# Optimization experiments

Measured on AMD Instinct MI355X. Metric: run time of the kernel, lower is better.

The kernel has to match this reference:

```python
import jax, jax.numpy as jnp
import numpy as np

N = 8192
E = 524288
IN_DIM = 128
HID = 256
OUT_DIM = 128
N_LAYERS = 3
N_HEADS = 4
HEAD_DIM = HID // N_HEADS


def setup_inputs() -> dict:
    key = jax.random.key(0)
    ks = jax.random.split(key, 12)
    s = 0.05
    return {
        "x": jax.random.normal(ks[0], (N, IN_DIM), dtype=jnp.float32),
        "edge_index": jax.random.randint(ks[1], (2, E), 0, N, dtype=jnp.int64),
        "W_in": jax.random.normal(ks[2], (HID, IN_DIM), dtype=jnp.float32) * s,
        "b_in": jnp.zeros((HID,), dtype=jnp.float32),
        "plasticity": jnp.ones((N_LAYERS,), dtype=jnp.float32),
        "synaptic": jnp.ones((N_LAYERS,), dtype=jnp.float32),
        "in_proj_w": jax.random.normal(ks[3], (3 * HID, HID), dtype=jnp.float32) * s,
        "in_proj_b": jnp.zeros((3 * HID,), dtype=jnp.float32),
        "out_proj_w": jax.random.normal(ks[4], (HID, HID), dtype=jnp.float32) * s,
        "out_proj_b": jnp.zeros((HID,), dtype=jnp.float32),
        "W_out": jax.random.normal(ks[5], (OUT_DIM, HID), dtype=jnp.float32) * s,
        "b_out": jnp.zeros((OUT_DIM,), dtype=jnp.float32),
    }


def _forward(x, edge_index, W_in, b_in, plasticity, synaptic,
             in_proj_w, in_proj_b, out_proj_w, out_proj_b, W_out, b_out):
    src, dst = edge_index[0], edge_index[1]  # x_j = x[src], aggregate at dst (source_to_target)
    x = x @ W_in.T + b_in  # [N, HID]
    for i in range(N_LAYERS):
        x = x * jax.nn.sigmoid(plasticity[i])
        # message: x_j * sigmoid(synaptic) (scalar edge weight); aggr='add'
        agg = jax.ops.segment_sum(x[src], dst, num_segments=N)  # gather-scatter-add
        x = jax.nn.leaky_relu(agg * jax.nn.sigmoid(synaptic[i]), negative_slope=0.01)
    # MultiheadAttention over all N nodes (seq_len=N, batch=1)
    qkv = x @ in_proj_w.T + in_proj_b  # [N, 3*HID]
    q, k, v = jnp.split(qkv, 3, axis=-1)
    q = q.reshape(N, N_HEADS, HEAD_DIM).transpose(1, 0, 2)  # [h, n, d]
    k = k.reshape(N, N_HEADS, HEAD_DIM).transpose(1, 0, 2)
    v = v.reshape(N, N_HEADS, HEAD_DIM).transpose(1, 0, 2)
    scores = jnp.einsum("hnd,hmd->hnm", q, k) / np.sqrt(HEAD_DIM).astype(np.float32)
    attn = jax.nn.softmax(scores, axis=-1)
    o = jnp.einsum("hnm,hmd->hnd", attn, v)  # [h, n, d]
    o = o.transpose(1, 0, 2).reshape(N, HID)
    x = o @ out_proj_w.T + out_proj_b
    return x @ W_out.T + b_out  # [N, OUT_DIM]


def reference(x, edge_index, W_in, b_in, plasticity, synaptic,
              in_proj_w, in_proj_b, out_proj_w, out_proj_b, W_out, b_out):
    return _forward(x, edge_index, W_in, b_in, plasticity, synaptic,
                    in_proj_w, in_proj_b, out_proj_w, out_proj_b, W_out, b_out)
```

## Files before the change

### kernel.cpp

```cpp
#include <hip/hip_runtime.h>
#include <hip/hip_bf16.h>
#include <float.h>

#define N_NODES 8192
#define NEDGE   524288
#define IND     128
#define HID     256
#define OUTD    128
#define NHEAD   4
#define HD      64

typedef short short8 __attribute__((ext_vector_type(8)));
typedef short short4v __attribute__((ext_vector_type(4)));
typedef float f32x4  __attribute__((ext_vector_type(4)));
typedef float f32x16 __attribute__((ext_vector_type(16)));
typedef unsigned int u32x4 __attribute__((ext_vector_type(4)));

__device__ __forceinline__ float sigmoidf_(float x) { return 1.0f / (1.0f + expf(-x)); }

__device__ __forceinline__ unsigned short f2bf(float f) {
    __hip_bfloat16 b = __float2bfloat16(f);
    return __builtin_bit_cast(unsigned short, b);
}
__device__ __forceinline__ float bf2f(unsigned short u) {
    __hip_bfloat16 b = __builtin_bit_cast(__hip_bfloat16, u);
    return __bfloat162float(b);
}
__device__ __forceinline__ void split3(float x, unsigned short& a, unsigned short& b, unsigned short& c) {
    a = f2bf(x); float r = x - bf2f(a);
    b = f2bf(r); r = r - bf2f(b);
    c = f2bf(r);
}
__device__ __forceinline__ void split2(float x, unsigned short& a, unsigned short& b) {
    a = f2bf(x); float r = x - bf2f(a);
    b = f2bf(r);
}
__device__ __forceinline__ unsigned int cvtpk(float lo, float hi) {
    unsigned int r;
    asm("v_cvt_pk_bf16_f32 %0, %1, %2" : "=v"(r) : "v"(lo), "v"(hi));
    return r;
}
__device__ __forceinline__ void plswap(unsigned int& a, unsigned int& b) {
    asm volatile("v_permlane32_swap_b32 %0, %1" : "+v"(a), "+v"(b));
}
__device__ __forceinline__ void gll16(const void* g, void* l) {
    __builtin_amdgcn_global_load_lds(
        (const __attribute__((address_space(1))) void*)g,
        (__attribute__((address_space(3))) void*)l, 16, 0, 0);
}
__device__ __forceinline__ f32x16 mfma32(short8 a, short8 b, f32x16 c) {
    return __builtin_amdgcn_mfma_f32_32x32x16_bf16(a, b, c, 0, 0, 0);
}

__global__ void hist_kernel(const int* __restrict__ ei, int* __restrict__ deg)
{
    int e = blockIdx.x * blockDim.x + threadIdx.x;
    if (e < NEDGE) atomicAdd(&deg[ei[NEDGE + e]], 1);
}

__global__ __launch_bounds__(1024) void scan_kernel(
    const int* __restrict__ deg, int* __restrict__ row_ptr, int* __restrict__ cursor)
{
    __shared__ int sh[1024];
    const int t = threadIdx.x;
    int v[8]; int s = 0;
    #pragma unroll
    for (int i = 0; i < 8; ++i) { v[i] = deg[t * 8 + i]; s += v[i]; }
    sh[t] = s; __syncthreads();
    for (int off = 1; off < 1024; off <<= 1) {
        int add = (t >= off) ? sh[t - off] : 0;
        __syncthreads();
        sh[t] += add;
        __syncthreads();
    }
    int base = sh[t] - s;
    #pragma unroll
    for (int i = 0; i < 8; ++i) {
        row_ptr[t * 8 + i] = base;
        cursor[t * 8 + i]  = base;
        base += v[i];
    }
    if (t == 1023) row_ptr[N_NODES] = base;
}

__global__ void scatter_kernel(const int* __restrict__ ei, int* __restrict__ cursor,
                               int* __restrict__ esrc)
{
    int e = blockIdx.x * blockDim.x + threadIdx.x;
    if (e < NEDGE) {
        int d = ei[NEDGE + e];
        int p = atomicAdd(&cursor[d], 1);
        esrc[p] = ei[e];
    }
}

__global__ __launch_bounds__(256) void split_x_kernel(
    const float* __restrict__ x,
    unsigned short* __restrict__ X0, unsigned short* __restrict__ X1,
    unsigned short* __restrict__ X2)
{
    const int i = (blockIdx.x * 256 + threadIdx.x) * 8;
    float4 a = *(const float4*)(x + i);
    float4 b = *(const float4*)(x + i + 4);
    float v[8] = {a.x, a.y, a.z, a.w, b.x, b.y, b.z, b.w};
    short8 c0, c1, c2;
    #pragma unroll
    for (int j = 0; j < 8; ++j) {
        unsigned short p, q, r;
        split3(v[j], p, q, r);
        c0[j] = (short)p; c1[j] = (short)q; c2[j] = (short)r;
    }
    *(short8*)(X0 + i) = c0;
    *(short8*)(X1 + i) = c1;
    *(short8*)(X2 + i) = c2;
}

__global__ __launch_bounds__(256) void aggregate_kernel(
    const float* __restrict__ hin, float* __restrict__ hout,
    const int* __restrict__ row_ptr, const int* __restrict__ esrc,
    const float* __restrict__ plas, const float* __restrict__ syn, int layer)
{
    const int b = blockIdx.x;
    const int c = threadIdx.x;
    const int st = row_ptr[b], en = row_ptr[b + 1];
    float a0 = 0.f, a1 = 0.f, a2 = 0.f, a3 = 0.f;
    int e = st;
    for (; e + 4 <= en; e += 4) {
        int s0 = esrc[e], s1 = esrc[e + 1], s2 = esrc[e + 2], s3 = esrc[e + 3];
        a0 += hin[(size_t)s0 * HID + c];
        a1 += hin[(size_t)s1 * HID + c];
        a2 += hin[(size_t)s2 * HID + c];
        a3 += hin[(size_t)s3 * HID + c];
    }
    float acc = (a0 + a1) + (a2 + a3);
    for (; e < en; ++e) acc += hin[(size_t)esrc[e] * HID + c];
    const float scale = sigmoidf_(plas[layer]) * sigmoidf_(syn[layer]);
    float x = acc * scale;
    hout[(size_t)b * HID + c] = (x > 0.f) ? x : 0.01f * x;
}

__global__ __launch_bounds__(256) void aggregate_split_kernel(
    const float* __restrict__ hin,
    unsigned short* __restrict__ H0, unsigned short* __restrict__ H1,
    unsigned short* __restrict__ H2,
    const int* __restrict__ row_ptr, const int* __restrict__ esrc,
    const float* __restrict__ plas, const float* __restrict__ syn, int layer)
{
    const int b = blockIdx.x;
    const int c = threadIdx.x;
    const int st = row_ptr[b], en = row_ptr[b + 1];
    float a0 = 0.f, a1 = 0.f, a2 = 0.f, a3 = 0.f;
    int e = st;
    for (; e + 4 <= en; e += 4) {
        int s0 = esrc[e], s1 = esrc[e + 1], s2 = esrc[e + 2], s3 = esrc[e + 3];
        a0 += hin[(size_t)s0 * HID + c];
        a1 += hin[(size_t)s1 * HID + c];
        a2 += hin[(size_t)s2 * HID + c];
        a3 += hin[(size_t)s3 * HID + c];
    }
    float acc = (a0 + a1) + (a2 + a3);
    for (; e < en; ++e) acc += hin[(size_t)esrc[e] * HID + c];
    const float scale = sigmoidf_(plas[layer]) * sigmoidf_(syn[layer]);
    float x = acc * scale;
    x = (x > 0.f) ? x : 0.01f * x;
    unsigned short p, q, r;
    split3(x, p, q, r);
    H0[(size_t)b * HID + c] = p;
    H1[(size_t)b * HID + c] = q;
    H2[(size_t)b * HID + c] = r;
}

template<int NT, int NA, bool SOUT>
__global__ __launch_bounds__(256) void mfma_gemm_kernel(
    const unsigned short* __restrict__ A0, const unsigned short* __restrict__ A1,
    const unsigned short* __restrict__ A2,
    const float* __restrict__ W, const float* __restrict__ bias,
    float* __restrict__ Cf, unsigned short* __restrict__ C0, unsigned short* __restrict__ C1,
    int M, int Nn, int K)
{
    const int t = threadIdx.x;
    const int wv = t >> 6, lane = t & 63;
    const int l31 = lane & 31, l5 = lane >> 5;
    const int wm = wv & 1, wn = wv >> 1;
    const int m0 = blockIdx.x * 64 + wm * 32;
    const int n0 = blockIdx.y * 64 + wn * 32;
    const int mrow = m0 + l31;
    const int nrow = n0 + l31;

    f32x16 o;
    #pragma unroll
    for (int r = 0; r < 16; ++r) o[r] = 0.f;

    for (int k = 0; k < K; k += 16) {
        const int kk = k + l5 * 8;
        short8 af[NA];
        af[0] = *(const short8*)(A0 + (size_t)mrow * K + kk);
        af[1] = *(const short8*)(A1 + (size_t)mrow * K + kk);
        if (NA > 2) af[2] = *(const short8*)(A2 + (size_t)mrow * K + kk);
        const float* wp = W + (size_t)nrow * K + kk;
        float4 w4a = *(const float4*)wp, w4b = *(const float4*)(wp + 4);
        float wvle[8] = {w4a.x, w4a.y, w4a.z, w4a.w, w4b.x, w4b.y, w4b.z, w4b.w};
        short8 wf[3];
        #pragma unroll
        for (int j = 0; j < 8; ++j) {
            if (NT == 6) {
                unsigned short a, b, c;
                split3(wvle[j], a, b, c);
                wf[0][j] = (short)a; wf[1][j] = (short)b; wf[2][j] = (short)c;
            } else {
                unsigned short a, b;
                split2(wvle[j], a, b);
                wf[0][j] = (short)a; wf[1][j] = (short)b;
            }
        }
        if (NT == 6) {
            o = mfma32(wf[0], af[2], o);
            o = mfma32(wf[1], af[1], o);
            o = mfma32(wf[2], af[0], o);
            o = mfma32(wf[0], af[1], o);
            o = mfma32(wf[1], af[0], o);
            o = mfma32(wf[0], af[0], o);
        } else {
            o = mfma32(wf[0], af[1], o);
            o = mfma32(wf[1], af[0], o);
            o = mfma32(wf[0], af[0], o);
        }
    }

    #pragma unroll
    for (int g = 0; g < 4; ++g) {
        const int nb = n0 + g * 8 + l5 * 4;
        const float4 b4 = *(const float4*)(bias + nb);
        float v0 = o[4 * g + 0] + b4.x;
        float v1 = o[4 * g + 1] + b4.y;
        float v2 = o[4 * g + 2] + b4.z;
        float v3 = o[4 * g + 3] + b4.w;
        if (!SOUT) {
            float4 st = {v0, v1, v2, v3};
            *(float4*)(Cf + (size_t)mrow * Nn + nb) = st;
        } else {
            unsigned short h0, h1, p0, p1, q0, q1, r0, r1;
            split2(v0, h0, h1); split2(v1, p0, p1);
            split2(v2, q0, q1); split2(v3, r0, r1);
            short4v s0 = {(short)h0, (short)p0, (short)q0, (short)r0};
            short4v s1 = {(short)h1, (short)p1, (short)q1, (short)r1};
            *(short4v*)(C0 + (size_t)mrow * Nn + nb) = s0;
            *(short4v*)(C1 + (size_t)mrow * Nn + nb) = s1;
        }
    }
}

__global__ __launch_bounds__(256) void split_kernel(
    const float* __restrict__ qkv,
    unsigned short* __restrict__ Kc0, unsigned short* __restrict__ Kc1,
    unsigned short* __restrict__ Kc2, unsigned short* __restrict__ Vt0)
{
    __shared__ unsigned short vts[64 * 80];
    const int h  = blockIdx.y;
    const int n0 = blockIdx.x * 64;
    const int t  = threadIdx.x;
    const int r  = t >> 2;
    const int n  = n0 + r;
    const int dc = (t & 3) * 16;

    {
        const float* kp = qkv + (size_t)n * 768 + 256 + h * 64 + dc;
        float kv[16];
        #pragma unroll
        for (int i = 0; i < 16; i += 4) {
            float4 f = *(const float4*)(kp + i);
            kv[i] = f.x; kv[i+1] = f.y; kv[i+2] = f.z; kv[i+3] = f.w;
        }
        #pragma unroll
        for (int half = 0; half < 2; ++half) {
            short8 c0, c1, c2;
            #pragma unroll
            for (int j = 0; j < 8; ++j) {
                unsigned short a, b, c;
                split3(kv[half * 8 + j], a, b, c);
                c0[j] = (short)a; c1[j] = (short)b; c2[j] = (short)c;
            }
            const int pos = ((dc >> 3) + half) ^ (n & 7);
            const size_t base = ((size_t)(h * 8192 + n)) * 64 + pos * 8;
            *(short8*)(Kc0 + base) = c0;
            *(short8*)(Kc1 + base) = c1;
            *(short8*)(Kc2 + base) = c2;
        }
    }
    {
        const float* vp = qkv + (size_t)n * 768 + 512 + h * 64 + dc;
        #pragma unroll
        for (int i = 0; i < 16; i += 4) {
            float4 f = *(const float4*)(vp + i);
            float vv[4] = {f.x, f.y, f.z, f.w};
            #pragma unroll
            for (int k2 = 0; k2 < 4; ++k2)
                vts[(dc + i + k2) * 80 + r] = f2bf(vv[k2]);
        }
    }
    __syncthreads();
    #pragma unroll
    for (int i = 0; i < 2; ++i) {
        const int q = t * 2 + i;
        const int d = q >> 3, nc = q & 7;
        const int g = nc >> 2, c = nc & 3;
        short8 vv = *(const short8*)(&vts[d * 80 + nc * 8]);
        const size_t dst = ((size_t)(h * 64 + d)) * 8192 + n0 + g * 32 + ((c ^ (d & 3)) * 8);
        *(short8*)(Vt0 + dst) = vv;
    }
}

__global__ __launch_bounds__(256, 3) void attn_mfma_kernel(
    const float* __restrict__ qkv,
    const unsigned short* __restrict__ Kc0, const unsigned short* __restrict__ Kc1,
    const unsigned short* __restrict__ Kc2, const unsigned short* __restrict__ Vt0,
    unsigned short* __restrict__ Op16, float* __restrict__ Ml)
{
    __shared__ __align__(16) char smem[32768];
    const int h    = blockIdx.y;
    const int quar = blockIdx.z;
    const int n0   = blockIdx.x * 128;
    const int t    = threadIdx.x;
    const int wv   = t >> 6;
    const int lane = t & 63;
    const int l31  = lane & 31, l5 = lane >> 5;
    const int qbase = n0 + wv * 32;

    const float QSC = 0.125f * 1.4426950408889634f;
    short8 qf[3][4];
    #pragma unroll
    for (int ks = 0; ks < 4; ++ks) {
        const float* qp = qkv + (size_t)(qbase + l31) * 768 + h * 64 + ks * 16 + l5 * 8;
        float4 qa = *(const float4*)qp, qb4 = *(const float4*)(qp + 4);
        float qv[8] = {qa.x, qa.y, qa.z, qa.w, qb4.x, qb4.y, qb4.z, qb4.w};
        #pragma unroll
        for (int j = 0; j < 8; ++j) {
            unsigned short a, b, c;
            split3(qv[j] * QSC, a, b, c);
            qf[0][ks][j] = (short)a;
            qf[1][ks][j] = (short)b;
            qf[2][ks][j] = (short)c;
        }
    }

    const char* sgb[4];
    int ldso[4];
    #pragma unroll
    for (int i = 0; i < 4; ++i) {
        const int s = wv * 4 + i;
        if (s < 12) {
            const int c = s >> 2, rb = s & 3;
            const unsigned short* base = (c == 0) ? Kc0 : (c == 1) ? Kc1 : Kc2;
            const int row = rb * 8 + (lane >> 3);
            sgb[i] = (const char*)(base + ((size_t)(h * 8192 + quar * 2048 + row)) * 64 + (lane & 7) * 8);
            ldso[i] = c * 4096 + rb * 1024;
        } else {
            const int v = s - 12;
            const int d = v * 16 + (lane >> 2);
            sgb[i] = (const char*)(Vt0 + ((size_t)(h * 64 + d)) * 8192 + quar * 2048 + (lane & 3) * 8);
            ldso[i] = 12288 + v * 1024;
        }
    }
    const size_t ktstride = (wv < 3) ? 4096 : 64;

    auto STAGE = [&](int kt, int bb) {
        #pragma unroll
        for (int i = 0; i < 4; ++i)
            gll16(sgb[i] + (size_t)kt * ktstride, &smem[bb * 16384 + ldso[i]]);
    };

    f32x16 o[2];
    #pragma unroll
    for (int db = 0; db < 2; ++db)
        #pragma unroll
        for (int r = 0; r < 16; ++r) o[db][r] = 0.f;
    float mr = -FLT_MAX, ls = 0.f;

    STAGE(0, 0);
    __syncthreads();

    for (int kt = 0; kt < 64; ++kt) {
        const int bb = kt & 1;
        if (kt < 63) STAGE(kt + 1, bb ^ 1);
        const char* buf = &smem[bb * 16384];

        f32x16 s;
        #pragma unroll
        for (int r = 0; r < 16; ++r) s[r] = 0.f;

        __builtin_amdgcn_s_setprio(1);
        #pragma unroll
        for (int ks = 0; ks < 4; ++ks) {
            const int off = l31 * 128 + (((ks * 2 + l5) ^ (l31 & 7)) * 16);
            short8 k0 = *(const short8*)(buf + off);
            short8 k1 = *(const short8*)(buf + 4096 + off);
            short8 k2 = *(const short8*)(buf + 8192 + off);
            s = mfma32(k0, qf[2][ks], s);
            s = mfma32(k1, qf[1][ks], s);
            s = mfma32(k2, qf[0][ks], s);
            s = mfma32(k0, qf[1][ks], s);
            s = mfma32(k1, qf[0][ks], s);
            s = mfma32(k0, qf[0][ks], s);
        }
        __builtin_amdgcn_s_setprio(0);

        float mx = s[0];
        #pragma unroll
        for (int r = 1; r < 16; ++r) mx = fmaxf(mx, s[r]);
        mx = fmaxf(mx, __shfl_xor(mx, 32));
        if (__any(mx > mr + 12.0f)) {
            const float mn = fmaxf(mr, mx);
            const float alpha = exp2f(mr - mn);
            mr = mn;
            ls *= alpha;
            o[0] *= alpha;
            o[1] *= alpha;
        }
        float ps = 0.f;
        #pragma unroll
        for (int r = 0; r < 16; ++r) {
            float p = exp2f(s[r] - mr);
            s[r] = p;
            ps += p;
        }
        ps += __shfl_xor(ps, 32);
        ls += ps;

        short8 pb[2];
        #pragma unroll
        for (int ks = 0; ks < 2; ++ks) {
            const int rb = ks * 8;
            unsigned int A0 = cvtpk(s[rb + 0], s[rb + 1]);
            unsigned int A1 = cvtpk(s[rb + 2], s[rb + 3]);
            unsigned int B0 = cvtpk(s[rb + 4], s[rb + 5]);
            unsigned int B1 = cvtpk(s[rb + 6], s[rb + 7]);
            plswap(A0, B0);
            plswap(A1, B1);
            u32x4 pw; pw[0] = A0; pw[1] = A1; pw[2] = B0; pw[3] = B1;
            pb[ks] = __builtin_bit_cast(short8, pw);
        }

        __builtin_amdgcn_s_setprio(1);
        #pragma unroll
        for (int ks = 0; ks < 2; ++ks) {
            #pragma unroll
            for (int db = 0; db < 2; ++db) {
                const int d = db * 32 + l31;
                const int off = 12288 + d * 64 + (((ks * 2 + l5) ^ (d & 3)) * 16);
                short8 v = *(const short8*)(buf + off);
                o[db] = mfma32(v, pb[ks], o[db]);
            }
        }
        __builtin_amdgcn_s_setprio(0);

        __syncthreads();
    }

    {
        const int q = qbase + l31;
        unsigned short* opq = Op16 + ((size_t)((quar * 4 + h) * 8192 + q)) * 64;
        #pragma unroll
        for (int db = 0; db < 2; ++db) {
            #pragma unroll
            for (int tq = 0; tq < 4; ++tq) {
                const int d0 = db * 32 + tq * 8 + l5 * 4;
                unsigned int w0 = cvtpk(o[db][4 * tq + 0], o[db][4 * tq + 1]);
                unsigned int w1 = cvtpk(o[db][4 * tq + 2], o[db][4 * tq + 3]);
                uint2 st = {w0, w1};
                *(uint2*)(opq + d0) = st;
            }
        }
        if (l5 == 0) {
            Ml[((size_t)(quar * 4 + h) * 2 + 0) * 8192 + q] = mr;
            Ml[((size_t)(quar * 4 + h) * 2 + 1) * 8192 + q] = ls;
        }
    }
}

__global__ __launch_bounds__(256) void combine_kernel(
    const unsigned short* __restrict__ Op16, const float* __restrict__ Ml,
    unsigned short* __restrict__ aO0, unsigned short* __restrict__ aO1)
{
    const int idx = blockIdx.x * 256 + threadIdx.x;
    const int c = idx & 3;
    const int q = (idx >> 2) & 8191;
    const int h = idx >> 15;
    float m[4], l[4];
    float mg = -FLT_MAX;
    #pragma unroll
    for (int s = 0; s < 4; ++s) {
        m[s] = Ml[((size_t)(s * 4 + h) * 2 + 0) * 8192 + q];
        l[s] = Ml[((size_t)(s * 4 + h) * 2 + 1) * 8192 + q];
        mg = fmaxf(mg, m[s]);
    }
    float w[4], denom = 0.f;
    #pragma unroll
    for (int s = 0; s < 4; ++s) {
        w[s] = exp2f(m[s] - mg);
        denom += l[s] * w[s];
    }
    const float inv = 1.f / denom;
    float acc[16] = {};
    #pragma unroll
    for (int s = 0; s < 4; ++s) {
        const unsigned short* p = Op16 + ((size_t)(s * 4 + h) * 8192 + q) * 64 + c * 16;
        short8 v0 = *(const short8*)(p);
        short8 v1 = *(const short8*)(p + 8);
        #pragma unroll
        for (int i = 0; i < 8; ++i) {
            acc[i]     += w[s] * bf2f((unsigned short)v0[i]);
            acc[i + 8] += w[s] * bf2f((unsigned short)v1[i]);
        }
    }
    unsigned short* d0 = aO0 + (size_t)q * 256 + h * 64 + c * 16;
    unsigned short* d1 = aO1 + (size_t)q * 256 + h * 64 + c * 16;
    short8 o0, o1;
    #pragma unroll
    for (int i = 0; i < 8; ++i) {
        unsigned short a, b;
        split2(acc[i] * inv, a, b);
        o0[i] = (short)a; o1[i] = (short)b;
    }
    *(short8*)(d0) = o0;
    *(short8*)(d1) = o1;
    #pragma unroll
    for (int i = 0; i < 8; ++i) {
        unsigned short a, b;
        split2(acc[i + 8] * inv, a, b);
        o0[i] = (short)a; o1[i] = (short)b;
    }
    *(short8*)(d0 + 8) = o0;
    *(short8*)(d1 + 8) = o1;
}

extern "C" void kernel_launch(void* const* d_in, const int* in_sizes, int n_in,
                              void* d_out, int out_size, void* d_ws, size_t ws_size,
                              hipStream_t stream)
{
    const float* x     = (const float*)d_in[0];
    const int*   ei    = (const int*)  d_in[1];
    const float* W_in  = (const float*)d_in[2];
    const float* b_in  = (const float*)d_in[3];
    const float* plas  = (const float*)d_in[4];
    const float* syn   = (const float*)d_in[5];
    const float* inpw  = (const float*)d_in[6];
    const float* inpb  = (const float*)d_in[7];
    const float* outpw = (const float*)d_in[8];
    const float* outpb = (const float*)d_in[9];
    const float* Wout  = (const float*)d_in[10];
    const float* bout  = (const float*)d_in[11];
    float* out = (float*)d_out;

    char* ws = (char*)d_ws;
    float* h    = (float*)(ws + 0);
    float* h2   = (float*)(ws + (8u  << 20));
    float* qkv  = (float*)(ws + (16u << 20));
    unsigned short* xc0  = (unsigned short*)(ws + (16u << 20));
    unsigned short* xc1  = (unsigned short*)(ws + (18u << 20));
    unsigned short* xc2  = (unsigned short*)(ws + (20u << 20));
    unsigned short* h2c0 = (unsigned short*)(ws + (8u  << 20));
    unsigned short* h2c1 = (unsigned short*)(ws + (12u << 20));
    unsigned short* h2c2 = (unsigned short*)(ws + (40u << 20));
    unsigned short* Kc0  = (unsigned short*)(ws + 0);
    unsigned short* Kc1  = (unsigned short*)(ws + (4u  << 20));
    unsigned short* Kc2  = (unsigned short*)(ws + (8u  << 20));
    unsigned short* Vt0  = (unsigned short*)(ws + (12u << 20));
    unsigned short* Op16 = (unsigned short*)(ws + (40u << 20));
    unsigned short* aOc0 = (unsigned short*)(ws + 0);
    unsigned short* aOc1 = (unsigned short*)(ws + (4u  << 20));
    unsigned short* tmpc0 = (unsigned short*)(ws + (8u  << 20));
    unsigned short* tmpc1 = (unsigned short*)(ws + (12u << 20));
    int*   rowp = (int*)(ws + (56u << 20));
    int*   curs = (int*)(ws + (56u << 20) + 40960);
    int*   esrc = (int*)(ws + (56u << 20) + 81920);
    float* Ml   = (float*)(ws + (56u << 20) + 81920);

    hipMemsetAsync(curs, 0, N_NODES * sizeof(int), stream);
    hist_kernel<<<NEDGE / 256, 256, 0, stream>>>(ei, curs);
    scan_kernel<<<1, 1024, 0, stream>>>(curs, rowp, curs);
    scatter_kernel<<<NEDGE / 256, 256, 0, stream>>>(ei, curs, esrc);

    split_x_kernel<<<(N_NODES * IND) / (256 * 8), 256, 0, stream>>>(x, xc0, xc1, xc2);
    mfma_gemm_kernel<6, 3, false><<<dim3(N_NODES / 64, HID / 64), 256, 0, stream>>>(
        xc0, xc1, xc2, W_in, b_in, h, nullptr, nullptr, N_NODES, HID, IND);

    aggregate_kernel<<<N_NODES, 256, 0, stream>>>(h,  h2, rowp, esrc, plas, syn, 0);
    aggregate_kernel<<<N_NODES, 256, 0, stream>>>(h2, h,  rowp, esrc, plas, syn, 1);
    aggregate_split_kernel<<<N_NODES, 256, 0, stream>>>(h, h2c0, h2c1, h2c2,
                                                        rowp, esrc, plas, syn, 2);

    mfma_gemm_kernel<6, 3, false><<<dim3(N_NODES / 64, 768 / 64), 256, 0, stream>>>(
        h2c0, h2c1, h2c2, inpw, inpb, qkv, nullptr, nullptr, N_NODES, 768, HID);

    split_kernel<<<dim3(N_NODES / 64, NHEAD), 256, 0, stream>>>(
        qkv, Kc0, Kc1, Kc2, Vt0);

    attn_mfma_kernel<<<dim3(N_NODES / 128, NHEAD, 4), 256, 0, stream>>>(
        qkv, Kc0, Kc1, Kc2, Vt0, Op16, Ml);

    combine_kernel<<<512, 256, 0, stream>>>(Op16, Ml, aOc0, aOc1);

    mfma_gemm_kernel<3, 2, true><<<dim3(N_NODES / 64, HID / 64), 256, 0, stream>>>(
        aOc0, aOc1, nullptr, outpw, outpb, nullptr, tmpc0, tmpc1, N_NODES, HID, HID);
    mfma_gemm_kernel<3, 2, false><<<dim3(N_NODES / 64, OUTD / 64), 256, 0, stream>>>(
        tmpc0, tmpc1, nullptr, Wout, bout, out, nullptr, nullptr, N_NODES, OUTD, HID);
}
```

Before: 602.7 us.

## Pre-split weights into bf16 parts, slice aggregation by column, hoist attention offsets

Weights are now split once into bf16 hi/mid/lo planes by a dedicated kernel before each GEMM, so GEMM blocks stop re-splitting fp32 weights inside the K loop. The aggregation kernels remap blocks so each block handles 4 destination nodes over a 64-column slice, with blocks interleaved across halves of the node range, aiming for better cache locality on gathers. The attention kernel precomputes swizzled LDS offsets outside its loop and raises the launch-bounds occupancy hint from 3 to 4, which may increase register pressure. Extra small split launches are added and the split planes use extra workspace regions.

```diff
diff --git a/kernel.cpp b/kernel.cpp
--- a/kernel.cpp
+++ b/kernel.cpp
@@ -94,14 +94,13 @@
     }
 }
 
-__global__ __launch_bounds__(256) void split_x_kernel(
-    const float* __restrict__ x,
-    unsigned short* __restrict__ X0, unsigned short* __restrict__ X1,
-    unsigned short* __restrict__ X2)
+__global__ __launch_bounds__(256) void split_w_kernel(
+    const float* __restrict__ w, unsigned short* __restrict__ Wc, int elems)
 {
     const int i = (blockIdx.x * 256 + threadIdx.x) * 8;
-    float4 a = *(const float4*)(x + i);
-    float4 b = *(const float4*)(x + i + 4);
+    if (i >= elems) return;
+    float4 a = *(const float4*)(w + i);
+    float4 b = *(const float4*)(w + i + 4);
     float v[8] = {a.x, a.y, a.z, a.w, b.x, b.y, b.z, b.w};
     short8 c0, c1, c2;
     #pragma unroll
@@ -110,36 +109,40 @@
         split3(v[j], p, q, r);
         c0[j] = (short)p; c1[j] = (short)q; c2[j] = (short)r;
     }
-    *(short8*)(X0 + i) = c0;
-    *(short8*)(X1 + i) = c1;
-    *(short8*)(X2 + i) = c2;
-}
-
-__global__ __launch_bounds__(256) void aggregate_kernel(
+    *(short8*)(Wc + i) = c0;
+    *(short8*)(Wc + elems + i) = c1;
+    *(short8*)(Wc + 2 * elems + i) = c2;
+}
+
+__global__ __launch_bounds__(256) void aggregate_sliced_kernel(
     const float* __restrict__ hin, float* __restrict__ hout,
     const int* __restrict__ row_ptr, const int* __restrict__ esrc,
     const float* __restrict__ plas, const float* __restrict__ syn, int layer)
 {
     const int b = blockIdx.x;
-    const int c = threadIdx.x;
-    const int st = row_ptr[b], en = row_ptr[b + 1];
+    const int xs = b & 7, g = b >> 3;
+    const int slice = xs & 3, halfn = xs >> 2;
+    const int t = threadIdx.x;
+    const int dst = halfn * 4096 + g * 4 + (t >> 6);
+    const int col = slice * 64 + (t & 63);
+    const int st = row_ptr[dst], en = row_ptr[dst + 1];
     float a0 = 0.f, a1 = 0.f, a2 = 0.f, a3 = 0.f;
     int e = st;
     for (; e + 4 <= en; e += 4) {
         int s0 = esrc[e], s1 = esrc[e + 1], s2 = esrc[e + 2], s3 = esrc[e + 3];
-        a0 += hin[(size_t)s0 * HID + c];
-        a1 += hin[(size_t)s1 * HID + c];
-        a2 += hin[(size_t)s2 * HID + c];
-        a3 += hin[(size_t)s3 * HID + c];
+        a0 += hin[(size_t)s0 * HID + col];
+        a1 += hin[(size_t)s1 * HID + col];
+        a2 += hin[(size_t)s2 * HID + col];
+        a3 += hin[(size_t)s3 * HID + col];
     }
     float acc = (a0 + a1) + (a2 + a3);
-    for (; e < en; ++e) acc += hin[(size_t)esrc[e] * HID + c];
+    for (; e < en; ++e) acc += hin[(size_t)esrc[e] * HID + col];
     const float scale = sigmoidf_(plas[layer]) * sigmoidf_(syn[layer]);
     float x = acc * scale;
-    hout[(size_t)b * HID + c] = (x > 0.f) ? x : 0.01f * x;
-}
-
-__global__ __launch_bounds__(256) void aggregate_split_kernel(
+    hout[(size_t)dst * HID + col] = (x > 0.f) ? x : 0.01f * x;
+}
+
+__global__ __launch_bounds__(256) void aggregate_sliced_split_kernel(
     const float* __restrict__ hin,
     unsigned short* __restrict__ H0, unsigned short* __restrict__ H1,
     unsigned short* __restrict__ H2,
@@ -147,34 +150,38 @@
     const float* __restrict__ plas, const float* __restrict__ syn, int layer)
 {
     const int b = blockIdx.x;
-    const int c = threadIdx.x;
-    const int st = row_ptr[b], en = row_ptr[b + 1];
+    const int xs = b & 7, g = b >> 3;
+    const int slice = xs & 3, halfn = xs >> 2;
+    const int t = threadIdx.x;
+    const int dst = halfn * 4096 + g * 4 + (t >> 6);
+    const int col = slice * 64 + (t & 63);
+    const int st = row_ptr[dst], en = row_ptr[dst + 1];
     float a0 = 0.f, a1 = 0.f, a2 = 0.f, a3 = 0.f;
     int e = st;
     for (; e + 4 <= en; e += 4) {
         int s0 = esrc[e], s1 = esrc[e + 1], s2 = esrc[e + 2], s3 = esrc[e + 3];
-        a0 += hin[(size_t)s0 * HID + c];
-        a1 += hin[(size_t)s1 * HID + c];
-        a2 += hin[(size_t)s2 * HID + c];
-        a3 += hin[(size_t)s3 * HID + c];
+        a0 += hin[(size_t)s0 * HID + col];
+        a1 += hin[(size_t)s1 * HID + col];
+        a2 += hin[(size_t)s2 * HID + col];
+        a3 += hin[(size_t)s3 * HID + col];
     }
     float acc = (a0 + a1) + (a2 + a3);
-    for (; e < en; ++e) acc += hin[(size_t)esrc[e] * HID + c];
+    for (; e < en; ++e) acc += hin[(size_t)esrc[e] * HID + col];
     const float scale = sigmoidf_(plas[layer]) * sigmoidf_(syn[layer]);
     float x = acc * scale;
     x = (x > 0.f) ? x : 0.01f * x;
     unsigned short p, q, r;
     split3(x, p, q, r);
-    H0[(size_t)b * HID + c] = p;
-    H1[(size_t)b * HID + c] = q;
-    H2[(size_t)b * HID + c] = r;
+    H0[(size_t)dst * HID + col] = p;
+    H1[(size_t)dst * HID + col] = q;
+    H2[(size_t)dst * HID + col] = r;
 }
 
 template<int NT, int NA, bool SOUT>
 __global__ __launch_bounds__(256) void mfma_gemm_kernel(
     const unsigned short* __restrict__ A0, const unsigned short* __restrict__ A1,
     const unsigned short* __restrict__ A2,
-    const float* __restrict__ W, const float* __restrict__ bias,
+    const unsigned short* __restrict__ Wc, const float* __restrict__ bias,
     float* __restrict__ Cf, unsigned short* __restrict__ C0, unsigned short* __restrict__ C1,
     int M, int Nn, int K)
 {
@@ -186,6 +193,7 @@
     const int n0 = blockIdx.y * 64 + wn * 32;
     const int mrow = m0 + l31;
     const int nrow = n0 + l31;
+    const size_t NK = (size_t)Nn * K;
 
     f32x16 o;
     #pragma unroll
@@ -197,33 +205,21 @@
         af[0] = *(const short8*)(A0 + (size_t)mrow * K + kk);
         af[1] = *(const short8*)(A1 + (size_t)mrow * K + kk);
         if (NA > 2) af[2] = *(const short8*)(A2 + (size_t)mrow * K + kk);
-        const float* wp = W + (size_t)nrow * K + kk;
-        float4 w4a = *(const float4*)wp, w4b = *(const float4*)(wp + 4);
-        float wvle[8] = {w4a.x, w4a.y, w4a.z, w4a.w, w4b.x, w4b.y, w4b.z, w4b.w};
-        short8 wf[3];
-        #pragma unroll
-        for (int j = 0; j < 8; ++j) {
-            if (NT == 6) {
-                unsigned short a, b, c;
-                split3(wvle[j], a, b, c);
-                wf[0][j] = (short)a; wf[1][j] = (short)b; wf[2][j] = (short)c;
-            } else {
-                unsigned short a, b;
-                split2(wvle[j], a, b);
-                wf[0][j] = (short)a; wf[1][j] = (short)b;
-            }
-        }
+        const unsigned short* wp = Wc + (size_t)nrow * K + kk;
+        short8 w0 = *(const short8*)(wp);
+        short8 w1 = *(const short8*)(wp + NK);
         if (NT == 6) {
-            o = mfma32(wf[0], af[2], o);
-            o = mfma32(wf[1], af[1], o);
-            o = mfma32(wf[2], af[0], o);
-            o = mfma32(wf[0], af[1], o);
-            o = mfma32(wf[1], af[0], o);
-            o = mfma32(wf[0], af[0], o);
+            short8 w2 = *(const short8*)(wp + 2 * NK);
+            o = mfma32(w0, af[2], o);
+            o = mfma32(w1, af[1], o);
+            o = mfma32(w2, af[0], o);
+            o = mfma32(w0, af[1], o);
+            o = mfma32(w1, af[0], o);
+            o = mfma32(w0, af[0], o);
         } else {
-            o = mfma32(wf[0], af[1], o);
-            o = mfma32(wf[1], af[0], o);
-            o = mfma32(wf[0], af[0], o);
+            o = mfma32(w0, af[1], o);
+            o = mfma32(w1, af[0], o);
+            o = mfma32(w0, af[0], o);
         }
     }
 
@@ -310,7 +306,7 @@
     }
 }
 
-__global__ __launch_bounds__(256, 3) void attn_mfma_kernel(
+__global__ __launch_bounds__(256, 4) void attn_mfma_kernel(
     const float* __restrict__ qkv,
     const unsigned short* __restrict__ Kc0, const unsigned short* __restrict__ Kc1,
     const unsigned short* __restrict__ Kc2, const unsigned short* __restrict__ Vt0,
@@ -342,6 +338,18 @@
             qf[2][ks][j] = (short)c;
         }
     }
+
+    int koff[4], voff[2][2];
+    #pragma unroll
+    for (int ks = 0; ks < 4; ++ks)
+        koff[ks] = l31 * 128 + (((ks * 2 + l5) ^ (l31 & 7)) * 16);
+    #pragma unroll
+    for (int ks = 0; ks < 2; ++ks)
+        #pragma unroll
+        for (int db = 0; db < 2; ++db) {
+            const int d = db * 32 + l31;
+            voff[ks][db] = 12288 + d * 64 + (((ks * 2 + l5) ^ (d & 3)) * 16);
+        }
 
     const char* sgb[4];
     int ldso[4];
@@ -391,7 +399,7 @@
         __builtin_amdgcn_s_setprio(1);
         #pragma unroll
         for (int ks = 0; ks < 4; ++ks) {
-            const int off = l31 * 128 + (((ks * 2 + l5) ^ (l31 & 7)) * 16);
+            const int off = koff[ks];
             short8 k0 = *(const short8*)(buf + off);
             short8 k1 = *(const short8*)(buf + 4096 + off);
             short8 k2 = *(const short8*)(buf + 8192 + off);
@@ -445,9 +453,7 @@
         for (int ks = 0; ks < 2; ++ks) {
             #pragma unroll
             for (int db = 0; db < 2; ++db) {
-                const int d = db * 32 + l31;
-                const int off = 12288 + d * 64 + (((ks * 2 + l5) ^ (d & 3)) * 16);
-                short8 v = *(const short8*)(buf + off);
+                short8 v = *(const short8*)(buf + voff[ks][db]);
                 o[db] = mfma32(v, pb[ks], o[db]);
             }
         }
@@ -561,6 +567,10 @@
     unsigned short* h2c0 = (unsigned short*)(ws + (8u  << 20));
     unsigned short* h2c1 = (unsigned short*)(ws + (12u << 20));
     unsigned short* h2c2 = (unsigned short*)(ws + (40u << 20));
+    unsigned short* Wic  = (unsigned short*)(ws + (44u << 20));
+    unsigned short* ipc  = (unsigned short*)(ws + (45u << 20));
+    unsigned short* opc  = (unsigned short*)(ws + (16u << 20));
+    unsigned short* woc  = (unsigned short*)(ws + (17u << 20));
     unsigned short* Kc0  = (unsigned short*)(ws + 0);
     unsigned short* Kc1  = (unsigned short*)(ws + (4u  << 20));
     unsigned short* Kc2  = (unsigned short*)(ws + (8u  << 20));
@@ -580,17 +590,21 @@
     scan_kernel<<<1, 1024, 0, stream>>>(curs, rowp, curs);
     scatter_kernel<<<NEDGE / 256, 256, 0, stream>>>(ei, curs, esrc);
 
-    split_x_kernel<<<(N_NODES * IND) / (256 * 8), 256, 0, stream>>>(x, xc0, xc1, xc2);
+    split_w_kernel<<<(HID * IND) / 2048, 256, 0, stream>>>(W_in, Wic, HID * IND);
+    split_w_kernel<<<(768 * HID) / 2048, 256, 0, stream>>>(inpw, ipc, 768 * HID);
+    split_w_kernel<<<(N_NODES * IND) / 2048, 256, 0, stream>>>(x, xc0, N_NODES * IND);
+
     mfma_gemm_kernel<6, 3, false><<<dim3(N_NODES / 64, HID / 64), 256, 0, stream>>>(
-        xc0, xc1, xc2, W_in, b_in, h, nullptr, nullptr, N_NODES, HID, IND);
-
-    aggregate_kernel<<<N_NODES, 256, 0, stream>>>(h,  h2, rowp, esrc, plas, syn, 0);
-    aggregate_kernel<<<N_NODES, 256, 0, stream>>>(h2, h,  rowp, esrc, plas, syn, 1);
-    aggregate_split_kernel<<<N_NODES, 256, 0, stream>>>(h, h2c0, h2c1, h2c2,
-                                                        rowp, esrc, plas, syn, 2);
+        xc0, xc0 + N_NODES * IND, xc0 + 2 * N_NODES * IND, Wic, b_in,
+        h, nullptr, nullptr, N_NODES, HID, IND);
+
+    aggregate_sliced_kernel<<<N_NODES, 256, 0, stream>>>(h,  h2, rowp, esrc, plas, syn, 0);
+    aggregate_sliced_kernel<<<N_NODES, 256, 0, stream>>>(h2, h,  rowp, esrc, plas, syn, 1);
+    aggregate_sliced_split_kernel<<<N_NODES, 256, 0, stream>>>(h, h2c0, h2c1, h2c2,
+                                                               rowp, esrc, plas, syn, 2);
 
     mfma_gemm_kernel<6, 3, false><<<dim3(N_NODES / 64, 768 / 64), 256, 0, stream>>>(
-        h2c0, h2c1, h2c2, inpw, inpb, qkv, nullptr, nullptr, N_NODES, 768, HID);
+        h2c0, h2c1, h2c2, ipc, inpb, qkv, nullptr, nullptr, N_NODES, 768, HID);
 
     split_kernel<<<dim3(N_NODES / 64, NHEAD), 256, 0, stream>>>(
         qkv, Kc0, Kc1, Kc2, Vt0);
@@ -600,8 +614,11 @@
 
     combine_kernel<<<512, 256, 0, stream>>>(Op16, Ml, aOc0, aOc1);
 
+    split_w_kernel<<<(HID * HID) / 2048, 256, 0, stream>>>(outpw, opc, HID * HID);
+    split_w_kernel<<<(OUTD * HID) / 2048, 256, 0, stream>>>(Wout, woc, OUTD * HID);
+
     mfma_gemm_kernel<3, 2, true><<<dim3(N_NODES / 64, HID / 64), 256, 0, stream>>>(
-        aOc0, aOc1, nullptr, outpw, outpb, nullptr, tmpc0, tmpc1, N_NODES, HID, HID);
+        aOc0, aOc1, nullptr, opc, outpb, nullptr, tmpc0, tmpc1, N_NODES, HID, HID);
     mfma_gemm_kernel<3, 2, false><<<dim3(N_NODES / 64, OUTD / 64), 256, 0, stream>>>(
-        tmpc0, tmpc1, nullptr, Wout, bout, out, nullptr, nullptr, N_NODES, OUTD, HID);
-}
+        tmpc0, tmpc1, nullptr, woc, bout, out, nullptr, nullptr, N_NODES, OUTD, HID);
+}
```

Result: no change. 613.1 us (+1.7%).
